# Performance work log

Measured on AMD Instinct MI355X. Metric: run time of the kernel, lower is better.

The kernel has to match this reference:

```python
import jax, jax.numpy as jnp
import numpy as np

# hyperparameters from __init__
MIN_ = 5000
MAX_ = 5000
MIN_P = 0.1
MAX_P = 0.2
EPS = 1e-8


def _gumbel_sample_mask(probs, cand_mask, k, key):
    """Weighted sampling without replacement of up to k items from the
    candidate set, via Gumbel-top-k. Returns a 0/1 float mask over the
    flattened map. Items outside cand_mask get score -inf; if fewer than k
    candidates exist, the -inf entries picked by top_k are masked out."""
    hw = probs.shape[0]
    logp = jnp.where(cand_mask, jnp.log(probs), -jnp.inf)
    u = jax.random.uniform(key, (hw,), minval=1e-12, maxval=1.0)
    scores = logp - jnp.log(-jnp.log(u))  # gumbel-perturbed log-probs
    top_scores, top_idx = jax.lax.top_k(scores, k)
    valid = jnp.isfinite(top_scores).astype(jnp.float32)
    # scatter with .max so invalid (-inf) slots write 0 harmlessly
    return jnp.zeros((hw,), jnp.float32).at[top_idx].max(valid)


def setup_inputs() -> dict:
    key = jax.random.key(0)
    k1, k2 = jax.random.split(key)
    cam = jax.random.uniform(k1, (4096, 4096), dtype=jnp.float32)
    roi = jax.random.randint(k2, (4096, 4096), 0, 2, dtype=jnp.int32)
    return {"cam": cam, "roi": roi}


def reference(cam, roi):
    h, w = cam.shape
    hw = h * w
    key = jax.random.key(42)
    k_fg, k_bg = jax.random.split(key)

    # ---- foreground capture (_ProbFG, seed_tech='weighted') ----
    roi_f = roi.astype(cam.dtype)
    cam_fg = (cam * roi_f + EPS).reshape(hw)
    n_fg = (MAX_P * jnp.sum(roi_f)).astype(jnp.int32)
    # stable descending sort -> top-n_fg candidate mask
    order_fg = jnp.argsort(-cam_fg)  # jnp.argsort is stable
    cand_fg = jnp.zeros((hw,), bool).at[order_fg].set(jnp.arange(hw) < n_fg)
    fg = _gumbel_sample_mask(cam_fg, cand_fg, MAX_, k_fg)

    # ---- background capture (_ProbBG, bg_seed_tech='weighted') ----
    cam_bg = (cam + EPS).reshape(hw)
    n_bg = int(MIN_P * hw)  # static
    order_bg = jnp.argsort(cam_bg)  # stable ascending
    cand_bg = jnp.zeros((hw,), bool).at[order_bg].set(jnp.arange(hw) < n_bg)
    probs_bg = jax.nn.relu(1.0 - cam_bg) + EPS
    bg = _gumbel_sample_mask(probs_bg, cand_bg, min(MIN_, n_bg), k_bg)

    return fg.reshape(h, w), bg.reshape(h, w)
```

## Files before the change

### kernel.cpp

```cpp
#include <hip/hip_runtime.h>
#include <math.h>
#include <stdint.h>

#define HW 16777216u
#define COL_CAP  65536u
#define LIST_CAP (4u*1024u*1024u)
#define WIN_CAP  8192u
#define STAGE_CAP 6144u

__host__ __device__ inline uint32_t tf_rotl(uint32_t x, int n){ return (x<<n)|(x>>(32-n)); }

__host__ __device__ inline void threefry2x32(uint32_t k0, uint32_t k1, uint32_t x0, uint32_t x1,
                                             uint32_t &o0, uint32_t &o1){
  uint32_t ks2 = k0 ^ k1 ^ 0x1BD11BDAu;
  x0 += k0; x1 += k1;
#define TF_R4(a,b,c,d) \
  x0 += x1; x1 = tf_rotl(x1,(a)); x1 ^= x0; \
  x0 += x1; x1 = tf_rotl(x1,(b)); x1 ^= x0; \
  x0 += x1; x1 = tf_rotl(x1,(c)); x1 ^= x0; \
  x0 += x1; x1 = tf_rotl(x1,(d)); x1 ^= x0;
  TF_R4(13,15,26,6)  x0 += k1;  x1 += ks2 + 1u;
  TF_R4(17,29,16,24) x0 += ks2; x1 += k0  + 2u;
  TF_R4(13,15,26,6)  x0 += k0;  x1 += k1  + 3u;
  TF_R4(17,29,16,24) x0 += k1;  x1 += ks2 + 4u;
  TF_R4(13,15,26,6)  x0 += ks2; x1 += k0  + 5u;
#undef TF_R4
  o0 = x0; o1 = x1;
}

__device__ __forceinline__ uint32_t okey(float f){
  uint32_t b = __float_as_uint(f);
  return (b & 0x80000000u) ? ~b : (b | 0x80000000u);
}
__device__ __forceinline__ float inv_okey(uint32_t k){
  uint32_t b = (k & 0x80000000u) ? (k & 0x7FFFFFFFu) : ~k;
  return __uint_as_float(b);
}

__device__ __forceinline__ unsigned vbin(float v){
  unsigned b = (unsigned)(v * 4096.0f);
  return b > 4095u ? 4095u : b;
}
__device__ __forceinline__ unsigned sbin(float s){
  float t = (s + 4.0f) * 51.2f;
  int b = (int)t;
  b = b < 0 ? 0 : (b > 1023 ? 1023 : b);
  return (unsigned)b;
}

__device__ __forceinline__ unsigned wave_reserve_lds(unsigned* cnt){
  unsigned long long m = __ballot(1);
  unsigned lane = threadIdx.x & 63u;
  unsigned leader = (unsigned)__ffsll((unsigned long long)m) - 1u;
  unsigned prefix = (unsigned)__popcll(m & ((1ull << lane) - 1ull));
  unsigned base = 0u;
  if (lane == leader) base = atomicAdd(cnt, (unsigned)__popcll(m));
  base = __shfl(base, (int)leader, 64);
  return base + prefix;
}

__device__ __forceinline__ float gumbel_u(uint32_t kk0, uint32_t kk1, uint32_t i){
  uint32_t y0, y1; threefry2x32(kk0, kk1, 0u, i, y0, y1);
  uint32_t bits = y0 ^ y1;
  float f = __uint_as_float((bits >> 9) | 0x3F800000u) - 1.0f;
  return fmaxf(1e-12f, f + 1e-12f);
}

__device__ __forceinline__ float gumbel_score(uint32_t kk0, uint32_t kk1, uint32_t i, float prob){
  float u = gumbel_u(kk0, kk1, i);
  float l1 = (float)log((double)u);
  float l2 = (float)log((double)(-l1));
  float lp = (float)log((double)prob);
  return lp - l2;
}



__global__ __launch_bounds__(1024) void k_hist_val(
    const float4* __restrict__ cam4, const int4* __restrict__ roi4,
    unsigned* __restrict__ h1a, unsigned* __restrict__ h1b,
    unsigned* __restrict__ st){
  __shared__ unsigned hp[4096];
  __shared__ unsigned ssum;
  for (int j = threadIdx.x; j < 4096; j += 1024) hp[j] = 0u;
  if (threadIdx.x == 0) ssum = 0u;
  __syncthreads();
  unsigned base = blockIdx.x * 8192u;
  unsigned rs = 0u;
  for (int j = 0; j < 8; j++){
    unsigned u = base + threadIdx.x + (unsigned)j*1024u;
    float4 c = cam4[u]; int4 r = roi4[u];
#define HV(cc, rr) { unsigned b = vbin((cc) + 1e-8f); \
    atomicAdd(&hp[b], (rr) ? 0x10001u : 1u); rs += (unsigned)(rr); }
    HV(c.x, r.x) HV(c.y, r.y) HV(c.z, r.z) HV(c.w, r.w)
#undef HV
  }
  for (int o = 32; o; o >>= 1) rs += __shfl_down(rs, o, 64);
  if ((threadIdx.x & 63u) == 0u) atomicAdd(&ssum, rs);
  __syncthreads();
  for (int j = threadIdx.x; j < 4096; j += 1024){
    unsigned p = hp[j];
    if (p){
      unsigned fa = p >> 16, fb = p & 0xFFFFu;
      if (fa) atomicAdd(&h1a[j], fa);
      if (fb) atomicAdd(&h1b[j], fb);
    }
  }
  if (threadIdx.x == 0) atomicAdd(&st[0], ssum);
}

template<int CPB>
__device__ void block_select_g(const unsigned* __restrict__ h, unsigned n, bool top,
                               unsigned* out_bin, unsigned* out_rem){
  __shared__ unsigned csum[256];
  __shared__ unsigned sb, sr;
  unsigned t = threadIdx.x;
  if (t < 256u){
    unsigned s = 0u;
    #pragma unroll
    for (int j = 0; j < CPB; j++) s += h[t*(unsigned)CPB + (unsigned)j];
    csum[t] = s;
  }
  __syncthreads();
  if (t < 64u){
    unsigned v[4]; unsigned s = 0u;
    #pragma unroll
    for (unsigned j = 0; j < 4u; j++){
      unsigned pos = t*4u + j;
      unsigned c = top ? 255u - pos : pos;
      v[j] = csum[c]; s += v[j];
    }
    unsigned incl = s;
    #pragma unroll
    for (int o = 1; o < 64; o <<= 1){
      unsigned u = __shfl_up(incl, o, 64);
      if ((int)t >= o) incl += u;
    }
    unsigned excl = incl - s;
    if (incl >= n && excl < n){
      unsigned rem = n - excl; unsigned c = 0u;
      #pragma unroll
      for (unsigned j = 0; j < 4u; j++){
        unsigned pos = t*4u + j; c = top ? 255u - pos : pos;
        if (v[j] >= rem) break; rem -= v[j];
      }
      if (CPB > 1){
        unsigned hv[CPB > 1 ? CPB : 1];
        #pragma unroll
        for (int j = 0; j < CPB; j++) hv[j] = h[c*(unsigned)CPB + (unsigned)j];
        int b;
        if (top){ for (b = CPB-1; b > 0; b--){ if (hv[b] >= rem) break; rem -= hv[b]; } }
        else    { for (b = 0; b < CPB-1; b++){ if (hv[b] >= rem) break; rem -= hv[b]; } }
        sb = c*(unsigned)CPB + (unsigned)b; sr = rem;
      } else {
        sb = c; sr = rem;
      }
    }
  }
  __syncthreads();
  *out_bin = sb; *out_rem = sr;
  __syncthreads();
}

__global__ __launch_bounds__(1024, 8) void k_collect_map(
    const float4* __restrict__ cam4, const int4* __restrict__ roi4,
    const unsigned* __restrict__ h1a, const unsigned* __restrict__ h1b,
    unsigned* __restrict__ st,
    unsigned long long* __restrict__ LA, unsigned long long* __restrict__ LB,
    unsigned long long* __restrict__ colA, unsigned long long* __restrict__ colB,
    unsigned* __restrict__ ccnt,
    unsigned* __restrict__ sh1a, unsigned* __restrict__ sh1b,
    uint32_t kf0, uint32_t kf1, uint32_t kb0, uint32_t kb1, float u_min){
  __shared__ unsigned long long bufA[2560], bufB[2560];
  __shared__ unsigned long long tieA[512], tieB[512];
  __shared__ unsigned la[1024], lb[1024];
  __shared__ unsigned nA_s, nB_s, tA_s, tB_s, bA_s, bB_s, gA_s, gB_s, kA_n, kB_n;
  unsigned selA, remA, selB, remB;
  unsigned nfg = (unsigned)(0.2f * (float)st[0]);
  block_select_g<16>(h1a, nfg, true, &selA, &remA);
  block_select_g<16>(h1b, 1677721u, false, &selB, &remB);
  if (blockIdx.x == 0 && threadIdx.x == 0){
    st[8] = selA; st[9] = remA; st[16] = selB; st[17] = remB;
  }
  if (threadIdx.x < 1024u){ la[threadIdx.x] = 0u; lb[threadIdx.x] = 0u; }
  if (threadIdx.x == 0){ nA_s = 0u; nB_s = 0u; tA_s = 0u; tB_s = 0u; }
  __syncthreads();
  unsigned base = blockIdx.x * 4096u;
  for (int j = 0; j < 4; j++){
    unsigned u = base + threadIdx.x + (unsigned)j*1024u;
    float4 c = cam4[u]; int4 r = roi4[u];
#define KM(cc, rr, kk) { unsigned i = 4u*u + (kk); \
    float vbg = (cc) + 1e-8f; \
    unsigned bb = vbin(vbg); \
    float vfg = (rr) ? vbg : 1e-8f; \
    unsigned bf = (rr) ? bb : 0u; \
    if (bf > selA){ unsigned p = wave_reserve_lds(&nA_s); \
      if (p < 2560u) bufA[p] = ((unsigned long long)__float_as_uint(vfg) << 32) | i; } \
    else if (bf == selA){ unsigned p = wave_reserve_lds(&tA_s); \
      if (p < 512u) tieA[p] = ((unsigned long long)okey(vfg) << 32) | i; } \
    if (bb < selB){ \
      float pb2 = fmaxf(1.0f - vbg, 0.0f) + 1e-8f; \
      unsigned p = wave_reserve_lds(&nB_s); \
      if (p < 2560u) bufB[p] = ((unsigned long long)__float_as_uint(pb2) << 32) | i; } \
    else if (bb == selB){ unsigned p = wave_reserve_lds(&tB_s); \
      if (p < 512u) tieB[p] = ((unsigned long long)okey(vbg) << 32) | i; } }
    KM(c.x, r.x, 0u) KM(c.y, r.y, 1u) KM(c.z, r.z, 2u) KM(c.w, r.w, 3u)
#undef KM
  }
  __syncthreads();
  if (threadIdx.x == 0){
    nA_s = nA_s < 2560u ? nA_s : 2560u;  nB_s = nB_s < 2560u ? nB_s : 2560u;
    tA_s = tA_s < 512u  ? tA_s : 512u;   tB_s = tB_s < 512u  ? tB_s : 512u;
    gA_s = atomicAdd(&ccnt[0], tA_s); gB_s = atomicAdd(&ccnt[1], tB_s);
    kA_n = 0u; kB_n = 0u;
  }
  __syncthreads();
  for (unsigned t = threadIdx.x; t < tA_s; t += 1024u)
    if (gA_s + t < COL_CAP) colA[gA_s + t] = tieA[t];
  for (unsigned t = threadIdx.x; t < tB_s; t += 1024u)
    if (gB_s + t < COL_CAP) colB[gB_s + t] = tieB[t];
  __syncthreads();
  for (unsigned e = threadIdx.x; e < nA_s; e += 1024u){
    unsigned long long v = bufA[e];
    if (gumbel_u(kf0, kf1, (unsigned)v) >= u_min){
      unsigned p = wave_reserve_lds(&kA_n);
      if (p < 512u) tieA[p] = v;
    }
  }
  for (unsigned e = threadIdx.x; e < nB_s; e += 1024u){
    unsigned long long v = bufB[e];
    if (gumbel_u(kb0, kb1, (unsigned)v) >= u_min){
      unsigned p = wave_reserve_lds(&kB_n);
      if (p < 512u) tieB[p] = v;
    }
  }
  __syncthreads();
  if (threadIdx.x == 0){
    kA_n = kA_n < 512u ? kA_n : 512u;  kB_n = kB_n < 512u ? kB_n : 512u;
    bA_s = atomicAdd(&st[48], kA_n); bB_s = atomicAdd(&st[49], kB_n);
  }
  __syncthreads();
  for (unsigned e = threadIdx.x; e < kA_n; e += 1024u){
    unsigned long long v = tieA[e];
    unsigned i = (unsigned)v;
    float prob = __uint_as_float((unsigned)(v >> 32));
    float s = gumbel_score(kf0, kf1, i, prob);
    unsigned p = bA_s + e;
    if (p < LIST_CAP) LA[p] = ((unsigned long long)okey(s) << 32) | i;
    atomicAdd(&la[sbin(s)], 1u);
  }
  for (unsigned e = threadIdx.x; e < kB_n; e += 1024u){
    unsigned long long v = tieB[e];
    unsigned i = (unsigned)v;
    float prob = __uint_as_float((unsigned)(v >> 32));
    float s = gumbel_score(kb0, kb1, i, prob);
    unsigned p = bB_s + e;
    if (p < LIST_CAP) LB[p] = ((unsigned long long)okey(s) << 32) | i;
    atomicAdd(&lb[sbin(s)], 1u);
  }
  __syncthreads();
  if (threadIdx.x < 1024u){
    unsigned va = la[threadIdx.x], vb = lb[threadIdx.x];
    if (va) atomicAdd(&sh1a[threadIdx.x], va);
    if (vb) atomicAdd(&sh1b[threadIdx.x], vb);
  }
}

__global__ __launch_bounds__(512) void k_fin3c(
    const unsigned long long* __restrict__ colA,
    const unsigned long long* __restrict__ colB,
    const unsigned* __restrict__ ccnt, unsigned* __restrict__ st,
    unsigned long long* __restrict__ LA, unsigned long long* __restrict__ LB,
    unsigned* __restrict__ sh1a, unsigned* __restrict__ sh1b,
    uint32_t kf0, uint32_t kf1, uint32_t kb0, uint32_t kb1, float u_min){
  __shared__ unsigned long long scol[STAGE_CAP];
  __shared__ unsigned long long app[1024];
  __shared__ unsigned eq[1024];
  __shared__ unsigned h[256];
  __shared__ unsigned eqn, s_pref, s_rem, napp, gbase, s_cut;
  for (int side = 0; side < 2; side++){
    const unsigned long long* col = side ? colB : colA;
    int base = side ? 16 : 8;
    bool top = (side == 0);
    unsigned m = ccnt[side]; if (m > COL_CAP) m = COL_CAP;
    unsigned n = st[base+1];
    bool staged = (m <= STAGE_CAP);
    if (staged){
      for (unsigned e = threadIdx.x; e < m; e += 512u) scol[e] = col[e];
    }
    const unsigned long long* cp = staged ? (const unsigned long long*)scol : col;
    if (threadIdx.x == 0){ s_pref = 0u; s_rem = n; napp = 0u; }
    __syncthreads();
    for (int r = 0; r < 4; r++){
      if (threadIdx.x < 256u) h[threadIdx.x] = 0u;
      __syncthreads();
      unsigned pref = s_pref;
      for (unsigned e = threadIdx.x; e < m; e += 512u){
        unsigned k = (unsigned)(cp[e] >> 32);
        bool act = (r == 0) || ((k >> (32 - 8*r)) == pref);
        if (act) atomicAdd(&h[(k >> (24 - 8*r)) & 0xFFu], 1u);
      }
      __syncthreads();
      unsigned pb, pr;
      block_select_g<1>(h, s_rem, top, &pb, &pr);
      if (threadIdx.x == 0){ s_pref = (s_pref << 8) | pb; s_rem = pr; }
      __syncthreads();
    }
    unsigned T = s_pref, remF = s_rem;
    if (threadIdx.x == 0) eqn = 0u;
    __syncthreads();
    for (unsigned e = threadIdx.x; e < m; e += 512u){
      unsigned long long v = cp[e];
      if ((unsigned)(v >> 32) == T){
        unsigned p = atomicAdd(&eqn, 1u);
        if (p < 1024u) eq[p] = (unsigned)v;
      }
    }
    __syncthreads();
    unsigned kq = eqn < 1024u ? eqn : 1024u;
    for (unsigned t = threadIdx.x; t < kq; t += 512u){
      unsigned idx = eq[t], rank = 0u;
      for (unsigned j = 0; j < kq; j++) if (eq[j] < idx) rank++;
      if (rank == remF - 1u){ st[base+4] = T; st[base+5] = idx; s_cut = idx; }
    }
    __syncthreads();
    unsigned cut = s_cut;
    for (unsigned e = threadIdx.x; e < m; e += 512u){
      unsigned long long v = cp[e];
      unsigned k = (unsigned)(v >> 32), i = (unsigned)v;
      bool pass = top ? (k > T || (k == T && i <= cut))
                      : (k < T || (k == T && i <= cut));
      if (pass){
        if (gumbel_u(side ? kb0 : kf0, side ? kb1 : kf1, i) >= u_min){
          unsigned p = wave_reserve_lds(&napp);
          if (p < 1024u) app[p] = v;
        }
      }
    }
    __syncthreads();
    if (threadIdx.x == 0){
      napp = napp < 1024u ? napp : 1024u;
      gbase = atomicAdd(&st[48 + side], napp);
    }
    __syncthreads();
    unsigned long long* L = side ? LB : LA;
    unsigned* sh = side ? sh1b : sh1a;
    for (unsigned t = threadIdx.x; t < napp; t += 512u){
      unsigned long long v = app[t];
      unsigned k = (unsigned)(v >> 32), i = (unsigned)v;
      float val = inv_okey(k);
      float prob = side ? (fmaxf(1.0f - val, 0.0f) + 1e-8f) : val;
      float s = gumbel_score(side ? kb0 : kf0, side ? kb1 : kf1, i, prob);
      unsigned p = gbase + t;
      if (p < LIST_CAP) L[p] = ((unsigned long long)okey(s) << 32) | i;
      atomicAdd(&sh[sbin(s)], 1u);
    }
    __syncthreads();
  }
}

__global__ __launch_bounds__(1024) void k_collect_win(
    const unsigned long long* __restrict__ LA, const unsigned long long* __restrict__ LB,
    const unsigned* __restrict__ sh1a, const unsigned* __restrict__ sh1b,
    unsigned* __restrict__ st,
    unsigned* __restrict__ winA, unsigned* __restrict__ winB,
    unsigned long long* __restrict__ wcolA, unsigned long long* __restrict__ wcolB,
    unsigned* __restrict__ ccnt){
  __shared__ unsigned long long tA[512], tB[512];
  __shared__ unsigned wA[256], wB[256];
  __shared__ unsigned nwA, nwB, ntA, ntB, bwA, bwB, btA, btB;
  unsigned selA, remA, selB, remB;
  block_select_g<4>(sh1a, 5000u, true, &selA, &remA);
  block_select_g<4>(sh1b, 5000u, true, &selB, &remB);
  if (blockIdx.x == 0 && threadIdx.x == 0){
    st[24] = selA; st[25] = remA; st[32] = selB; st[33] = remB;
  }
  if (threadIdx.x == 0){ nwA = 0u; nwB = 0u; ntA = 0u; ntB = 0u; }
  __syncthreads();
  unsigned mA = st[48] < LIST_CAP ? st[48] : LIST_CAP;
  unsigned mB = st[49] < LIST_CAP ? st[49] : LIST_CAP;
  unsigned tid = blockIdx.x*1024u + threadIdx.x;
  unsigned stride = gridDim.x*1024u;
  for (unsigned e = tid; e < mA; e += stride){
    unsigned long long v = LA[e];
    unsigned b = sbin(inv_okey((unsigned)(v >> 32)));
    if (b > selA){ unsigned p = wave_reserve_lds(&nwA); if (p < 256u) wA[p] = (unsigned)v; }
    else if (b == selA){ unsigned p = wave_reserve_lds(&ntA); if (p < 512u) tA[p] = v; }
  }
  for (unsigned e = tid; e < mB; e += stride){
    unsigned long long v = LB[e];
    unsigned b = sbin(inv_okey((unsigned)(v >> 32)));
    if (b > selB){ unsigned p = wave_reserve_lds(&nwB); if (p < 256u) wB[p] = (unsigned)v; }
    else if (b == selB){ unsigned p = wave_reserve_lds(&ntB); if (p < 512u) tB[p] = v; }
  }
  __syncthreads();
  if (threadIdx.x == 0){
    nwA = nwA < 256u ? nwA : 256u;  nwB = nwB < 256u ? nwB : 256u;
    ntA = ntA < 512u ? ntA : 512u;  ntB = ntB < 512u ? ntB : 512u;
    bwA = atomicAdd(&st[50], nwA); bwB = atomicAdd(&st[51], nwB);
    btA = atomicAdd(&ccnt[2], ntA); btB = atomicAdd(&ccnt[3], ntB);
  }
  __syncthreads();
  for (unsigned t = threadIdx.x; t < nwA; t += 1024u)
    if (bwA + t < WIN_CAP) winA[bwA + t] = wA[t];
  for (unsigned t = threadIdx.x; t < nwB; t += 1024u)
    if (bwB + t < WIN_CAP) winB[bwB + t] = wB[t];
  for (unsigned t = threadIdx.x; t < ntA; t += 1024u)
    if (btA + t < COL_CAP) wcolA[btA + t] = tA[t];
  for (unsigned t = threadIdx.x; t < ntB; t += 1024u)
    if (btB + t < COL_CAP) wcolB[btB + t] = tB[t];
}

__global__ __launch_bounds__(512) void k_fin3s(
    const unsigned long long* __restrict__ wcolA,
    const unsigned long long* __restrict__ wcolB,
    const unsigned* __restrict__ ccnt, unsigned* __restrict__ st,
    unsigned* __restrict__ winA, unsigned* __restrict__ winB){
  __shared__ unsigned long long scol[STAGE_CAP];
  __shared__ unsigned app[2048];
  __shared__ unsigned eq[1024];
  __shared__ unsigned h[256];
  __shared__ unsigned eqn, s_pref, s_rem, napp, gbase, s_cut;
  for (int side = 0; side < 2; side++){
    const unsigned long long* col = side ? wcolB : wcolA;
    int base = side ? 32 : 24;
    unsigned m = ccnt[2+side]; if (m > COL_CAP) m = COL_CAP;
    unsigned n = st[base+1];
    bool staged = (m <= STAGE_CAP);
    if (staged){
      for (unsigned e = threadIdx.x; e < m; e += 512u) scol[e] = col[e];
    }
    const unsigned long long* cp = staged ? (const unsigned long long*)scol : col;
    if (threadIdx.x == 0){ s_pref = 0u; s_rem = n; napp = 0u; }
    __syncthreads();
    for (int r = 0; r < 4; r++){
      if (threadIdx.x < 256u) h[threadIdx.x] = 0u;
      __syncthreads();
      unsigned pref = s_pref;
      for (unsigned e = threadIdx.x; e < m; e += 512u){
        unsigned k = (unsigned)(cp[e] >> 32);
        bool act = (r == 0) || ((k >> (32 - 8*r)) == pref);
        if (act) atomicAdd(&h[(k >> (24 - 8*r)) & 0xFFu], 1u);
      }
      __syncthreads();
      unsigned pb, pr;
      block_select_g<1>(h, s_rem, true, &pb, &pr);
      if (threadIdx.x == 0){ s_pref = (s_pref << 8) | pb; s_rem = pr; }
      __syncthreads();
    }
    unsigned T = s_pref, remF = s_rem;
    if (threadIdx.x == 0) eqn = 0u;
    __syncthreads();
    for (unsigned e = threadIdx.x; e < m; e += 512u){
      unsigned long long v = cp[e];
      if ((unsigned)(v >> 32) == T){
        unsigned p = atomicAdd(&eqn, 1u);
        if (p < 1024u) eq[p] = (unsigned)v;
      }
    }
    __syncthreads();
    unsigned kq = eqn < 1024u ? eqn : 1024u;
    for (unsigned t = threadIdx.x; t < kq; t += 512u){
      unsigned idx = eq[t], rank = 0u;
      for (unsigned j = 0; j < kq; j++) if (eq[j] < idx) rank++;
      if (rank == remF - 1u){ st[base+4] = T; st[base+5] = idx; s_cut = idx; }
    }
    __syncthreads();
    unsigned cut = s_cut;
    for (unsigned e = threadIdx.x; e < m; e += 512u){
      unsigned long long v = cp[e];
      unsigned k = (unsigned)(v >> 32), i = (unsigned)v;
      if (k > T || (k == T && i <= cut)){
        unsigned p = wave_reserve_lds(&napp);
        if (p < 2048u) app[p] = i;
      }
    }
    __syncthreads();
    if (threadIdx.x == 0){
      napp = napp < 2048u ? napp : 2048u;
      gbase = atomicAdd(&st[50 + side], napp);
    }
    __syncthreads();
    unsigned* win = side ? winB : winA;
    for (unsigned t = threadIdx.x; t < napp; t += 512u)
      if (gbase + t < WIN_CAP) win[gbase + t] = app[t];
    __syncthreads();
  }
}

__global__ __launch_bounds__(1024) void k_zero(float4* __restrict__ out4){
  unsigned tid = blockIdx.x*1024u + threadIdx.x;
  float4 z = {0.f, 0.f, 0.f, 0.f};
  for (int j = 0; j < 16; j++) out4[tid + (unsigned)j*524288u] = z;
}

__global__ void k_scatter(float* __restrict__ out,
                          const unsigned* __restrict__ winA, const unsigned* __restrict__ winB,
                          const unsigned* __restrict__ st){
  unsigned t = blockIdx.x*256u + threadIdx.x;
  unsigned nA = st[50] < WIN_CAP ? st[50] : WIN_CAP;
  unsigned nB = st[51] < WIN_CAP ? st[51] : WIN_CAP;
  if (t < nA) out[winA[t]] = 1.0f;
  if (t < nB) out[HW + winB[t]] = 1.0f;
}

extern "C" void kernel_launch(void* const* d_in, const int* in_sizes, int n_in,
                              void* d_out, int out_size, void* d_ws, size_t ws_size,
                              hipStream_t stream) {
  (void)in_sizes; (void)n_in; (void)out_size; (void)ws_size;
  const float4* cam4 = (const float4*)d_in[0];
  const int4*   roi4 = (const int4*)d_in[1];
  float* out = (float*)d_out;

  uint8_t* w = (uint8_t*)d_ws;
  unsigned* h1a  = (unsigned*)w;
  unsigned* h1b  = (unsigned*)(w + 16384);
  unsigned* sh1a = (unsigned*)(w + 32768);
  unsigned* sh1b = (unsigned*)(w + 36864);
  unsigned* ccnt = (unsigned*)(w + 40960);
  unsigned* st   = (unsigned*)(w + 41024);
  unsigned* winA = (unsigned*)(w + 41280);
  unsigned* winB = (unsigned*)(w + 74048);

  unsigned long long* LA    = (unsigned long long*)d_out;
  unsigned long long* LB    = (unsigned long long*)((uint8_t*)d_out + ((size_t)32<<20));
  unsigned long long* colA  = (unsigned long long*)((uint8_t*)d_out + ((size_t)64<<20));
  unsigned long long* colB  = colA + COL_CAP;
  unsigned long long* wcolA = colB + COL_CAP;
  unsigned long long* wcolB = wcolA + COL_CAP;

  uint32_t kf0,kf1,kb0,kb1;
  threefry2x32(0u, 42u, 0u, 0u, kf0, kf1);
  threefry2x32(0u, 42u, 0u, 1u, kb0, kb1);

  float u_min = nextafterf((float)exp(-exp(-(3.0 - 1e-7))), 0.0f);

  (void)hipMemsetAsync(w, 0, 41280, stream);

  k_hist_val<<<512, 1024, 0, stream>>>(cam4, roi4, h1a, h1b, st);
  k_collect_map<<<1024, 1024, 0, stream>>>(cam4, roi4, h1a, h1b, st, LA, LB,
                                           colA, colB, ccnt, sh1a, sh1b,
                                           kf0, kf1, kb0, kb1, u_min);
  k_fin3c<<<1, 512, 0, stream>>>(colA, colB, ccnt, st, LA, LB, sh1a, sh1b,
                                 kf0, kf1, kb0, kb1, u_min);
  k_collect_win<<<256, 1024, 0, stream>>>(LA, LB, sh1a, sh1b, st, winA, winB,
                                          wcolA, wcolB, ccnt);
  k_fin3s<<<1, 512, 0, stream>>>(wcolA, wcolB, ccnt, st, winA, winB);
  k_zero<<<512, 1024, 0, stream>>>((float4*)d_out);
  k_scatter<<<32, 256, 0, stream>>>(out, winA, winB, st);
}
```

Measured before the change: 363.2 us.

## Pack ROI into bitmask during histogram pass and reuse it in collect pass

The histogram kernel now packs the int32 ROI mask into 4-bit nibbles (one bit per element) and writes a compact bitmask to workspace. The collect kernel reads that bitmask instead of re-reading the full 64MB int32 ROI array, and its loads are hoisted ahead of the compute loop for more memory-level parallelism. When the workspace is large enough, scratch lists move from the output buffer into the workspace, so the output zeroing can use hipMemsetAsync. This relies on workspace size, and falls back to the old layout when the workspace is small.

Measured after the change: 362.0 us. No clear change (-0.3%).

```diff
diff --git a/kernel.cpp b/kernel.cpp
--- a/kernel.cpp
+++ b/kernel.cpp
@@ -79,8 +79,9 @@
 __global__ __launch_bounds__(1024) void k_hist_val(
     const float4* __restrict__ cam4, const int4* __restrict__ roi4,
     unsigned* __restrict__ h1a, unsigned* __restrict__ h1b,
-    unsigned* __restrict__ st){
+    unsigned* __restrict__ st, unsigned* __restrict__ roibits){
   __shared__ unsigned hp[4096];
+  __shared__ unsigned char nbuf[8192];
   __shared__ unsigned ssum;
   for (int j = threadIdx.x; j < 4096; j += 1024) hp[j] = 0u;
   if (threadIdx.x == 0) ssum = 0u;
@@ -90,6 +91,8 @@
   for (int j = 0; j < 8; j++){
     unsigned u = base + threadIdx.x + (unsigned)j*1024u;
     float4 c = cam4[u]; int4 r = roi4[u];
+    unsigned nib = (r.x ? 1u : 0u) | (r.y ? 2u : 0u) | (r.z ? 4u : 0u) | (r.w ? 8u : 0u);
+    nbuf[threadIdx.x + (unsigned)j*1024u] = (unsigned char)nib;
 #define HV(cc, rr) { unsigned b = vbin((cc) + 1e-8f); \
     atomicAdd(&hp[b], (rr) ? 0x10001u : 1u); rs += (unsigned)(rr); }
     HV(c.x, r.x) HV(c.y, r.y) HV(c.z, r.z) HV(c.w, r.w)
@@ -98,6 +101,16 @@
   for (int o = 32; o; o >>= 1) rs += __shfl_down(rs, o, 64);
   if ((threadIdx.x & 63u) == 0u) atomicAdd(&ssum, rs);
   __syncthreads();
+  {
+    const unsigned* nb32 = (const unsigned*)nbuf;
+    unsigned t = threadIdx.x;
+    unsigned w0 = nb32[2u*t], w1 = nb32[2u*t + 1u];
+    unsigned word =  (w0 & 0xFu)        | ((w0 >> 8) & 0xFu) << 4
+                  | ((w0 >> 16) & 0xFu) << 8  | ((w0 >> 24) & 0xFu) << 12
+                  |  (w1 & 0xFu) << 16  | ((w1 >> 8) & 0xFu) << 20
+                  | ((w1 >> 16) & 0xFu) << 24 | ((w1 >> 24) & 0xFu) << 28;
+    roibits[blockIdx.x*1024u + t] = word;
+  }
   for (int j = threadIdx.x; j < 4096; j += 1024){
     unsigned p = hp[j];
     if (p){
@@ -163,7 +176,7 @@
 }
 
 __global__ __launch_bounds__(1024, 8) void k_collect_map(
-    const float4* __restrict__ cam4, const int4* __restrict__ roi4,
+    const float4* __restrict__ cam4, const unsigned* __restrict__ roibits,
     const unsigned* __restrict__ h1a, const unsigned* __restrict__ h1b,
     unsigned* __restrict__ st,
     unsigned long long* __restrict__ LA, unsigned long long* __restrict__ LB,
@@ -186,14 +199,23 @@
   if (threadIdx.x == 0){ nA_s = 0u; nB_s = 0u; tA_s = 0u; tB_s = 0u; }
   __syncthreads();
   unsigned base = blockIdx.x * 4096u;
+  float4 pc[4]; unsigned pn[4];
+  #pragma unroll
   for (int j = 0; j < 4; j++){
     unsigned u = base + threadIdx.x + (unsigned)j*1024u;
-    float4 c = cam4[u]; int4 r = roi4[u];
-#define KM(cc, rr, kk) { unsigned i = 4u*u + (kk); \
+    pc[j] = cam4[u];
+    unsigned wrd = roibits[u >> 3];
+    pn[j] = (wrd >> ((u & 7u) * 4u)) & 0xFu;
+  }
+  #pragma unroll
+  for (int j = 0; j < 4; j++){
+    unsigned u = base + threadIdx.x + (unsigned)j*1024u;
+    float4 c = pc[j]; unsigned nib = pn[j];
+#define KM(cc, rn, kk) { unsigned i = 4u*u + (kk); \
     float vbg = (cc) + 1e-8f; \
     unsigned bb = vbin(vbg); \
-    float vfg = (rr) ? vbg : 1e-8f; \
-    unsigned bf = (rr) ? bb : 0u; \
+    float vfg = (rn) ? vbg : 1e-8f; \
+    unsigned bf = (rn) ? bb : 0u; \
     if (bf > selA){ unsigned p = wave_reserve_lds(&nA_s); \
       if (p < 2560u) bufA[p] = ((unsigned long long)__float_as_uint(vfg) << 32) | i; } \
     else if (bf == selA){ unsigned p = wave_reserve_lds(&tA_s); \
@@ -204,7 +226,7 @@
       if (p < 2560u) bufB[p] = ((unsigned long long)__float_as_uint(pb2) << 32) | i; } \
     else if (bb == selB){ unsigned p = wave_reserve_lds(&tB_s); \
       if (p < 512u) tieB[p] = ((unsigned long long)okey(vbg) << 32) | i; } }
-    KM(c.x, r.x, 0u) KM(c.y, r.y, 1u) KM(c.z, r.z, 2u) KM(c.w, r.w, 3u)
+    KM(c.x, (nib & 1u), 0u) KM(c.y, (nib & 2u), 1u) KM(c.z, (nib & 4u), 2u) KM(c.w, (nib & 8u), 3u)
 #undef KM
   }
   __syncthreads();
@@ -507,7 +529,7 @@
 extern "C" void kernel_launch(void* const* d_in, const int* in_sizes, int n_in,
                               void* d_out, int out_size, void* d_ws, size_t ws_size,
                               hipStream_t stream) {
-  (void)in_sizes; (void)n_in; (void)out_size; (void)ws_size;
+  (void)in_sizes; (void)n_in; (void)out_size;
   const float4* cam4 = (const float4*)d_in[0];
   const int4*   roi4 = (const int4*)d_in[1];
   float* out = (float*)d_out;
@@ -521,10 +543,13 @@
   unsigned* st   = (unsigned*)(w + 41024);
   unsigned* winA = (unsigned*)(w + 41280);
   unsigned* winB = (unsigned*)(w + 74048);
-
-  unsigned long long* LA    = (unsigned long long*)d_out;
-  unsigned long long* LB    = (unsigned long long*)((uint8_t*)d_out + ((size_t)32<<20));
-  unsigned long long* colA  = (unsigned long long*)((uint8_t*)d_out + ((size_t)64<<20));
+  unsigned* roibits = (unsigned*)(w + ((size_t)1<<20));
+
+  bool ws_big = ws_size >= ((size_t)80 << 20);
+  uint8_t* sc = ws_big ? (w + ((size_t)4 << 20)) : (uint8_t*)d_out;
+  unsigned long long* LA    = (unsigned long long*)sc;
+  unsigned long long* LB    = (unsigned long long*)(sc + ((size_t)32<<20));
+  unsigned long long* colA  = (unsigned long long*)(sc + ((size_t)64<<20));
   unsigned long long* colB  = colA + COL_CAP;
   unsigned long long* wcolA = colB + COL_CAP;
   unsigned long long* wcolB = wcolA + COL_CAP;
@@ -537,8 +562,8 @@
 
   (void)hipMemsetAsync(w, 0, 41280, stream);
 
-  k_hist_val<<<512, 1024, 0, stream>>>(cam4, roi4, h1a, h1b, st);
-  k_collect_map<<<1024, 1024, 0, stream>>>(cam4, roi4, h1a, h1b, st, LA, LB,
+  k_hist_val<<<512, 1024, 0, stream>>>(cam4, roi4, h1a, h1b, st, roibits);
+  k_collect_map<<<1024, 1024, 0, stream>>>(cam4, roibits, h1a, h1b, st, LA, LB,
                                            colA, colB, ccnt, sh1a, sh1b,
                                            kf0, kf1, kb0, kb1, u_min);
   k_fin3c<<<1, 512, 0, stream>>>(colA, colB, ccnt, st, LA, LB, sh1a, sh1b,
@@ -546,6 +571,7 @@
   k_collect_win<<<256, 1024, 0, stream>>>(LA, LB, sh1a, sh1b, st, winA, winB,
                                           wcolA, wcolB, ccnt);
   k_fin3s<<<1, 512, 0, stream>>>(wcolA, wcolB, ccnt, st, winA, winB);
-  k_zero<<<512, 1024, 0, stream>>>((float4*)d_out);
+  if (ws_big) (void)hipMemsetAsync(d_out, 0, (size_t)HW * 2u * sizeof(float), stream);
+  else        k_zero<<<512, 1024, 0, stream>>>((float4*)d_out);
   k_scatter<<<32, 256, 0, stream>>>(out, winA, winB, st);
 }
```
